# Performance work log

Hardware: AMD Instinct MI355X
Metric: run time of the kernel (lower is better)

The kernel has to match this reference:

```python
import jax, jax.numpy as jnp
import numpy as np

EPS = 1e-5
NEG = -1000000.0
H = 8

def layer_norm(v, g, b):
    mu = jnp.mean(v, axis=-1, keepdims=True)
    var = jnp.var(v, axis=-1, keepdims=True)
    return (v - mu) * jax.lax.rsqrt(var + EPS) * g + b

def setup_inputs() -> dict:
    key = jax.random.key(0)
    ks = jax.random.split(key, 12)
    B, T, Tc, D, Dc = 8, 2048, 512, 1024, 512
    s = lambda fan: 1.0 / np.sqrt(fan)
    return {
        'query': jax.random.normal(ks[0], (B, T, D), jnp.float32),
        'x': jax.random.normal(ks[1], (B, T, D), jnp.float32),
        'cond_emb': jax.random.normal(ks[2], (B, Tc, Dc), jnp.float32),
        'src_mask': jax.random.uniform(ks[3], (B, T, 1), jnp.float32),
        'cond_mask': jax.random.uniform(ks[4], (B, Tc, 1), jnp.float32),
        'norm_x_g': jnp.ones((D,), jnp.float32),
        'norm_x_b': jnp.zeros((D,), jnp.float32),
        'norm_c_g': jnp.ones((Dc,), jnp.float32),
        'norm_c_b': jnp.zeros((Dc,), jnp.float32),
        'W_kc': jax.random.normal(ks[5], (D, Dc), jnp.float32) * s(Dc),
        'b_kc': jnp.zeros((D,), jnp.float32),
        'W_vc': jax.random.normal(ks[6], (D, Dc), jnp.float32) * s(Dc),
        'b_vc': jnp.zeros((D,), jnp.float32),
        'W_kx': jax.random.normal(ks[7], (D, D), jnp.float32) * s(D),
        'b_kx': jnp.zeros((D,), jnp.float32),
        'W_vx': jax.random.normal(ks[8], (D, D), jnp.float32) * s(D),
        'b_vx': jnp.zeros((D,), jnp.float32),
        'W_y': jax.random.normal(ks[9], (D, D), jnp.float32) * s(D),
        'b_y': jnp.zeros((D,), jnp.float32),
    }

def reference(query, x, cond_emb, src_mask, cond_mask,
              norm_x_g, norm_x_b, norm_c_g, norm_c_b,
              W_kc, b_kc, W_vc, b_vc, W_kx, b_kx, W_vx, b_vx, W_y, b_y):
    B, T, D = x.shape
    Tc = cond_emb.shape[1]
    N = T + Tc
    xn = layer_norm(x, norm_x_g, norm_x_b)          # (B,T,D)
    cn = layer_norm(cond_emb, norm_c_g, norm_c_b)   # (B,Tc,Dc)
    # keys with additive mask penalty, concatenated over sequence dim
    k_cond = cn @ W_kc.T + b_kc + (1.0 - cond_mask) * NEG
    k_x = xn @ W_kx.T + b_kx + (1.0 - src_mask) * NEG
    key = jnp.concatenate([k_cond, k_x], axis=1)    # (B,N,D)
    q = jax.nn.softmax(query.reshape(B, T, H, D // H), axis=-1)
    k = jax.nn.softmax(key.reshape(B, N, H, D // H), axis=1)
    v_cond = (cn @ W_vc.T + b_vc) * cond_mask
    v_x = (xn @ W_vx.T + b_vx) * src_mask
    v = jnp.concatenate([v_cond, v_x], axis=1).reshape(B, N, H, D // H)
    attn = jnp.einsum('bnhd,bnhl->bhdl', k, v)      # (B,H,d,d) linear-attention KV
    y = jnp.einsum('bthd,bhdl->bthl', q, attn).reshape(B, T, D)
    return y @ W_y.T + b_y
```

## Files before the change

### kernel.cpp

```cpp
#include <hip/hip_runtime.h>


typedef short s16x8 __attribute__((ext_vector_type(8)));
typedef float f32x4 __attribute__((ext_vector_type(4)));

__device__ __forceinline__ float b2f(short s) {
    unsigned int u = ((unsigned int)(unsigned short)s) << 16;
    return __uint_as_float(u);
}
__device__ __forceinline__ short f2b(float f) {
    unsigned int u = __float_as_uint(f);
    u += 0x7fffu + ((u >> 16) & 1u);
    return (short)(u >> 16);
}

typedef void __attribute__((address_space(1)))* gas_ptr;
typedef void __attribute__((address_space(3)))* las_ptr;
__device__ __forceinline__ void async_cp16(const void* g, void* l) {
    __builtin_amdgcn_global_load_lds((gas_ptr)g, (las_ptr)l, 16, 0, 0);
}

__device__ __forceinline__ float pen_of(const float* __restrict__ cmask,
                                        const float* __restrict__ smask,
                                        int b, int n) {
    float mk = (n < 512) ? cmask[b * 512 + n] : smask[b * 2048 + n - 512];
    return (1.0f - mk) * -1000000.0f;
}

__global__ __launch_bounds__(256) void cvt_all(const float* __restrict__ Wkc,
                                               const float* __restrict__ Wvc,
                                               const float* __restrict__ Wkx,
                                               const float* __restrict__ Wvx,
                                               const float* __restrict__ Wy,
                                               short* __restrict__ dst) {
    int g = (blockIdx.x * 256 + threadIdx.x) * 4;
    const float* src;
    if (g < 524288)        src = Wkc + g;
    else if (g < 1048576)  src = Wvc + (g - 524288);
    else if (g < 2097152)  src = Wkx + (g - 1048576);
    else if (g < 3145728)  src = Wvx + (g - 2097152);
    else                   src = Wy  + (g - 3145728);
    float4 v = *(const float4*)src;
    short4 o;
    o.x = f2b(v.x); o.y = f2b(v.y); o.z = f2b(v.z); o.w = f2b(v.w);
    *(short4*)&dst[g] = o;
}

__global__ __launch_bounds__(256) void ln_kernel(const float* __restrict__ x,
                                                 const float* __restrict__ g,
                                                 const float* __restrict__ be,
                                                 short* __restrict__ out, int L) {
    long row = blockIdx.x;
    const float* xr = x + row * L;
    short* orow = out + row * L;
    int tid = threadIdx.x;
    int i0 = tid * 4;
    bool active = i0 < L;
    float v0 = 0.f, v1 = 0.f, v2 = 0.f, v3 = 0.f;
    if (active) {
        float4 p = *(const float4*)&xr[i0];
        v0 = p.x; v1 = p.y; v2 = p.z; v3 = p.w;
    }
    float s = v0 + v1 + v2 + v3;
    float s2 = v0*v0 + v1*v1 + v2*v2 + v3*v3;
    #pragma unroll
    for (int off = 32; off > 0; off >>= 1) {
        s  += __shfl_down(s, off);
        s2 += __shfl_down(s2, off);
    }
    __shared__ float ss[4], sq[4];
    int wave = tid >> 6, lane = tid & 63;
    if (lane == 0) { ss[wave] = s; sq[wave] = s2; }
    __syncthreads();
    if (tid == 0) {
        float t1 = ss[0] + ss[1] + ss[2] + ss[3];
        float t2 = sq[0] + sq[1] + sq[2] + sq[3];
        float mu = t1 / (float)L;
        float var = t2 / (float)L - mu * mu;
        ss[0] = mu;
        sq[0] = rsqrtf(var + 1e-5f);
    }
    __syncthreads();
    float mu = ss[0], rs = sq[0];
    if (active) {
        float4 gp = *(const float4*)&g[i0];
        float4 bp = *(const float4*)&be[i0];
        short4 o;
        o.x = f2b((v0 - mu) * rs * gp.x + bp.x);
        o.y = f2b((v1 - mu) * rs * gp.y + bp.y);
        o.z = f2b((v2 - mu) * rs * gp.z + bp.z);
        o.w = f2b((v3 - mu) * rs * gp.w + bp.w);
        *(short4*)&orow[i0] = o;
    }
}

__global__ __launch_bounds__(256) void qsoftmax_kernel(const float* __restrict__ q,
                                                       short* __restrict__ out) {
    long row = (long)blockIdx.x * 4 + (threadIdx.x >> 6);
    int lane = threadIdx.x & 63;
    const float* qr = q + row * 128;
    float2 p = *(const float2*)&qr[lane * 2];
    float v0 = p.x, v1 = p.y;
    float m = fmaxf(v0, v1);
    #pragma unroll
    for (int off = 32; off > 0; off >>= 1) m = fmaxf(m, __shfl_xor(m, off));
    float e0 = __expf(v0 - m), e1 = __expf(v1 - m);
    float s = e0 + e1;
    #pragma unroll
    for (int off = 32; off > 0; off >>= 1) s += __shfl_xor(s, off);
    float inv = 1.0f / s;
    short2 o; o.x = f2b(e0 * inv); o.y = f2b(e1 * inv);
    *(short2*)&out[row * 128 + lane * 2] = o;
}

__global__ __launch_bounds__(256) void kstats1(const short* __restrict__ klog,
                                               const float* __restrict__ cmask,
                                               const float* __restrict__ smask,
                                               float* __restrict__ partM,
                                               float* __restrict__ partS) {
    int c = blockIdx.x * 256 + threadIdx.x;
    int b = blockIdx.y;
    int n0 = blockIdx.z * 256;
    const short* base = klog + (long)b * 2560 * 1024 + c;
    float m = -3.4e38f, s = 0.f;
    for (int k = 0; k < 256; ++k) {
        int n = n0 + k;
        float v = b2f(base[(long)n * 1024]) + pen_of(cmask, smask, b, n);
        float nm = fmaxf(m, v);
        s = s * __expf(m - nm) + __expf(v - nm);
        m = nm;
    }
    long o = ((long)(b * 10 + blockIdx.z)) * 1024 + c;
    partM[o] = m;
    partS[o] = s;
}

__global__ __launch_bounds__(256) void kstats2(const float* __restrict__ partM,
                                               const float* __restrict__ partS,
                                               float* __restrict__ Ms,
                                               float* __restrict__ iSs) {
    int c = blockIdx.x * 256 + threadIdx.x;
    int b = blockIdx.y;
    float M = -3.4e38f;
    #pragma unroll
    for (int k = 0; k < 10; ++k)
        M = fmaxf(M, partM[((long)(b * 10 + k)) * 1024 + c]);
    float S = 0.f;
    #pragma unroll
    for (int k = 0; k < 10; ++k) {
        long o = ((long)(b * 10 + k)) * 1024 + c;
        S += partS[o] * __expf(partM[o] - M);
    }
    Ms[b * 1024 + c] = M;
    iSs[b * 1024 + c] = 1.0f / S;
}

template<int MODE>
__global__ __launch_bounds__(256) void gemm_bt(
        const short* __restrict__ A, int lda, long strideA,
        const short* __restrict__ B, int ldb,
        void* __restrict__ OutA, void* __restrict__ OutB,
        int ldo, long strideO,
        int K,
        const float* __restrict__ biasK, const float* __restrict__ biasV,
        const float* __restrict__ mask, long strideMask) {
    __shared__ short As[128 * 64];
    __shared__ short Bs[128 * 64];
    int tid = threadIdx.x;
    int wave = tid >> 6, lane = tid & 63;
    int n0 = blockIdx.x * 128;
    int m0 = blockIdx.y * 128;
    int z = blockIdx.z;

    const short* Ab;
    const short* Bb;
    if (MODE == 2) {
        Ab = A + (z & 7) * 128;
        Bb = B + (long)z * 16384;
    } else if (MODE == 4) {
        Ab = A + (long)z * strideA;
        Bb = B + (long)z * 1048576;
    } else {
        Ab = A + (long)z * strideA;
        Bb = B;
    }

    f32x4 acc[4][4];
    #pragma unroll
    for (int i = 0; i < 4; ++i)
        #pragma unroll
        for (int j = 0; j < 4; ++j) {
            f32x4 zz = {0.f, 0.f, 0.f, 0.f};
            acc[i][j] = zz;
        }

    int wm = wave >> 1, wn = wave & 1;
    int r = lane & 15, q = lane >> 4;

    for (int k0 = 0; k0 < K; k0 += 64) {
        __syncthreads();
        #pragma unroll
        for (int it = 0; it < 4; ++it) {
            int cid = it * 256 + tid;
            int row = cid >> 3;
            int c8  = cid & 7;
            int col = ((c8 ^ (row & 7)) << 3);
            const short* ga = Ab + (long)(m0 + row) * lda + k0 + col;
            const short* gb = Bb + (long)(n0 + row) * ldb + k0 + col;
            async_cp16(ga, &As[cid * 8]);
            async_cp16(gb, &Bs[cid * 8]);
        }
        __syncthreads();
        #pragma unroll
        for (int kk = 0; kk < 64; kk += 32) {
            s16x8 af[4], bfr[4];
            #pragma unroll
            for (int i = 0; i < 4; ++i) {
                int rowA = wm * 64 + i * 16 + r;
                int rowB = wn * 64 + i * 16 + r;
                int ch = (kk >> 3) + q;
                af[i]  = *(const s16x8*)&As[rowA * 64 + ((ch ^ (rowA & 7)) << 3)];
                bfr[i] = *(const s16x8*)&Bs[rowB * 64 + ((ch ^ (rowB & 7)) << 3)];
            }
            #pragma unroll
            for (int i = 0; i < 4; ++i)
                #pragma unroll
                for (int j = 0; j < 4; ++j)
                    acc[i][j] = __builtin_amdgcn_mfma_f32_16x16x32_bf16(af[i], bfr[j], acc[i][j], 0, 0, 0);
        }
    }

    #pragma unroll
    for (int i = 0; i < 4; ++i) {
        int gmb = m0 + wm * 64 + i * 16 + q * 4;
        #pragma unroll
        for (int j = 0; j < 4; ++j) {
            int gn = n0 + wn * 64 + j * 16 + r;
            #pragma unroll
            for (int rg = 0; rg < 4; ++rg) {
                int row = gmb + rg;
                float v = acc[i][j][rg];
                if (MODE == 0) {
                    if (gn < 1024) {
                        ((short*)OutA)[(long)z * strideO + (long)row * ldo + gn] =
                            f2b(v + biasK[gn]);
                    } else {
                        int gv = gn - 1024;
                        float mk = mask[(long)z * strideMask + row];
                        ((short*)OutB)[(long)z * strideO + (long)row * ldo + gv] =
                            f2b((v + biasV[gv]) * mk);
                    }
                } else if (MODE == 2) {
                    ((short*)OutA)[(long)(z >> 3) * 1048576 + (long)row * 1024 +
                                   (z & 7) * 128 + gn] = f2b(v);
                } else {
                    ((float*)OutA)[(long)z * strideO + (long)row * ldo + gn] =
                        v + biasK[gn];
                }
            }
        }
    }
}

template<int MODE>
__global__ __launch_bounds__(512, 2) void gemm256(
        const short* __restrict__ A, int lda, long strideA,
        const short* __restrict__ B, int ldb,
        void* __restrict__ OutA, void* __restrict__ OutB,
        int ldo, long strideO,
        int K,
        const float* __restrict__ biasK, const float* __restrict__ biasV,
        const float* __restrict__ mask, long strideMask) {
    extern __shared__ short lds[];
    int tid = threadIdx.x;
    int wave = tid >> 6, lane = tid & 63;
    int n0 = blockIdx.x * 256;
    int m0 = blockIdx.y * 256;
    int z = blockIdx.z;

    const short* Ab;
    const short* Bb;
    if (MODE == 4) {
        Ab = A + (long)z * strideA;
        Bb = B + (long)z * 1048576;
    } else {
        Ab = A + (long)z * strideA;
        Bb = B;
    }

    f32x4 acc[8][4];
    #pragma unroll
    for (int i = 0; i < 8; ++i)
        #pragma unroll
        for (int j = 0; j < 4; ++j) {
            f32x4 zz = {0.f, 0.f, 0.f, 0.f};
            acc[i][j] = zz;
        }

    int wm = wave >> 2, wn = wave & 3;
    int r = lane & 15, q = lane >> 4;

    auto stage = [&](int buf, int k0) {
        short* dstb = lds + buf * 32768;
        #pragma unroll
        for (int it = 0; it < 8; ++it) {
            int cid = it * 512 + tid;
            int rid = cid & 2047;
            int row = rid >> 3;
            int c8  = rid & 7;
            int col = ((c8 ^ (row & 7)) << 3);
            const short* g = (cid < 2048)
                ? (Ab + (long)(m0 + row) * lda + k0 + col)
                : (Bb + (long)(n0 + row) * ldb + k0 + col);
            async_cp16(g, dstb + cid * 8);
        }
    };

    auto compute = [&](int buf) {
        const short* Asb = lds + buf * 32768;
        const short* Bsb = Asb + 16384;
        s16x8 bfr[2][4];
        #pragma unroll
        for (int kk2 = 0; kk2 < 2; ++kk2)
            #pragma unroll
            for (int j = 0; j < 4; ++j) {
                int rowB = wn * 64 + j * 16 + r;
                int ch = kk2 * 4 + q;
                bfr[kk2][j] = *(const s16x8*)&Bsb[rowB * 64 + ((ch ^ (rowB & 7)) << 3)];
            }
        __builtin_amdgcn_s_setprio(1);
        #pragma unroll
        for (int i = 0; i < 8; ++i) {
            int rowA = wm * 128 + i * 16 + r;
            s16x8 a0 = *(const s16x8*)&Asb[rowA * 64 + (((q    ) ^ (rowA & 7)) << 3)];
            s16x8 a1 = *(const s16x8*)&Asb[rowA * 64 + (((q + 4) ^ (rowA & 7)) << 3)];
            #pragma unroll
            for (int j = 0; j < 4; ++j)
                acc[i][j] = __builtin_amdgcn_mfma_f32_16x16x32_bf16(a0, bfr[0][j], acc[i][j], 0, 0, 0);
            #pragma unroll
            for (int j = 0; j < 4; ++j)
                acc[i][j] = __builtin_amdgcn_mfma_f32_16x16x32_bf16(a1, bfr[1][j], acc[i][j], 0, 0, 0);
        }
        __builtin_amdgcn_s_setprio(0);
    };

    int nt = K >> 6;
    stage(0, 0);
    __syncthreads();
    for (int t = 0; t < nt; ++t) {
        if (t + 1 < nt) stage((t + 1) & 1, (t + 1) << 6);
        compute(t & 1);
        __syncthreads();
    }

    #pragma unroll
    for (int i = 0; i < 8; ++i) {
        int gmb = m0 + wm * 128 + i * 16 + q * 4;
        #pragma unroll
        for (int j = 0; j < 4; ++j) {
            int gn = n0 + wn * 64 + j * 16 + r;
            #pragma unroll
            for (int rg = 0; rg < 4; ++rg) {
                int row = gmb + rg;
                float v = acc[i][j][rg];
                if (MODE == 0) {
                    if (gn < 1024) {
                        ((short*)OutA)[(long)z * strideO + (long)row * ldo + gn] =
                            f2b(v + biasK[gn]);
                    } else {
                        int gv = gn - 1024;
                        float mk = mask[(long)z * strideMask + row];
                        ((short*)OutB)[(long)z * strideO + (long)row * ldo + gv] =
                            f2b((v + biasV[gv]) * mk);
                    }
                } else {
                    ((float*)OutA)[(long)z * strideO + (long)row * ldo + gn] =
                        v + biasK[gn];
                }
            }
        }
    }
}

__global__ __launch_bounds__(256) void attn_part(const short* __restrict__ klog,
                                                 const short* __restrict__ vbuf,
                                                 const float* __restrict__ cmask,
                                                 const float* __restrict__ smask,
                                                 const float* __restrict__ Ms,
                                                 float* __restrict__ pbuf) {
    __shared__ short kT[128 * 64];
    __shared__ short vT[128 * 64];
    int ns = blockIdx.x;
    int z = blockIdx.y;
    int b = z >> 3, h = z & 7;
    int tid = threadIdx.x;
    int wave = tid >> 6, lane = tid & 63;
    int r = lane & 15, q = lane >> 4;
    int wm = wave >> 1, wn = wave & 1;

    int cg = h * 128 + lane * 2;
    float M0 = Ms[b * 1024 + cg];
    float M1 = Ms[b * 1024 + cg + 1];

    f32x4 acc[4][4];
    #pragma unroll
    for (int i = 0; i < 4; ++i)
        #pragma unroll
        for (int j = 0; j < 4; ++j) {
            f32x4 zz = {0.f, 0.f, 0.f, 0.f};
            acc[i][j] = zz;
        }

    long base = ((long)b * 2560) * 1024 + h * 128;
    int nbase = ns * 320;
    int swz = (lane & 7) << 3;
    for (int n0 = 0; n0 < 320; n0 += 64) {
        __syncthreads();
        #pragma unroll 4
        for (int i = 0; i < 16; ++i) {
            int nl = i * 4 + wave;
            int n = nbase + n0 + nl;
            float pen = pen_of(cmask, smask, b, n);
            long g = base + (long)n * 1024 + lane * 2;
            short2 k2 = *(const short2*)&klog[g];
            short2 v2 = *(const short2*)&vbuf[g];
            float w0 = __expf(b2f(k2.x) + pen - M0);
            float w1 = __expf(b2f(k2.y) + pen - M1);
            int c = lane * 2;
            int sw = nl ^ swz;
            kT[c * 64 + sw] = f2b(w0);
            kT[(c + 1) * 64 + sw] = f2b(w1);
            vT[c * 64 + sw] = v2.x;
            vT[(c + 1) * 64 + sw] = v2.y;
        }
        __syncthreads();
        #pragma unroll
        for (int kk = 0; kk < 64; kk += 32) {
            s16x8 af[4], bfr[4];
            #pragma unroll
            for (int i = 0; i < 4; ++i) {
                int cA = wm * 64 + i * 16 + r;
                int cB = wn * 64 + i * 16 + r;
                af[i]  = *(const s16x8*)&kT[cA * 64 + ((kk + q * 8) ^ (((cA >> 1) & 7) << 3))];
                bfr[i] = *(const s16x8*)&vT[cB * 64 + ((kk + q * 8) ^ (((cB >> 1) & 7) << 3))];
            }
            #pragma unroll
            for (int i = 0; i < 4; ++i)
                #pragma unroll
                for (int j = 0; j < 4; ++j)
                    acc[i][j] = __builtin_amdgcn_mfma_f32_16x16x32_bf16(af[i], bfr[j], acc[i][j], 0, 0, 0);
        }
    }
    float* outp = pbuf + ((long)z * 8 + ns) * 16384;
    #pragma unroll
    for (int i = 0; i < 4; ++i) {
        int d0 = wm * 64 + i * 16 + q * 4;
        #pragma unroll
        for (int j = 0; j < 4; ++j) {
            int l = wn * 64 + j * 16 + r;
            *(f32x4*)&outp[l * 128 + d0] = acc[i][j];
        }
    }
}

__global__ __launch_bounds__(256) void reduce_attn(const float* __restrict__ pbuf,
                                                   const float* __restrict__ iSs,
                                                   short* __restrict__ attnD) {
    int idx = blockIdx.x * 256 + threadIdx.x;
    int z = idx >> 14, rem = idx & 16383;
    int d = rem & 127, l = rem >> 7;
    int b = z >> 3, h = z & 7;
    const float* p = pbuf + (long)z * 8 * 16384 + rem;
    float s = 0.f;
    #pragma unroll
    for (int ns = 0; ns < 8; ++ns) s += p[ns * 16384];
    attnD[(long)z * 16384 + d * 128 + l] = f2b(s * iSs[b * 1024 + h * 128 + d]);
}

extern "C" void kernel_launch(void* const* d_in, const int* in_sizes, int n_in,
                              void* d_out, int out_size, void* d_ws, size_t ws_size,
                              hipStream_t stream) {
    const float* query = (const float*)d_in[0];
    const float* x     = (const float*)d_in[1];
    const float* cond  = (const float*)d_in[2];
    const float* smask = (const float*)d_in[3];
    const float* cmask = (const float*)d_in[4];
    const float* gx  = (const float*)d_in[5];
    const float* bx  = (const float*)d_in[6];
    const float* gc  = (const float*)d_in[7];
    const float* bc  = (const float*)d_in[8];
    const float* Wkc = (const float*)d_in[9];
    const float* bkc = (const float*)d_in[10];
    const float* Wvc = (const float*)d_in[11];
    const float* bvc = (const float*)d_in[12];
    const float* Wkx = (const float*)d_in[13];
    const float* bkx = (const float*)d_in[14];
    const float* Wvx = (const float*)d_in[15];
    const float* bvx = (const float*)d_in[16];
    const float* Wy  = (const float*)d_in[17];
    const float* by  = (const float*)d_in[18];

    size_t o_xn    = 0;
    size_t o_cn    = o_xn    + 33554432;
    size_t o_klog  = o_cn    + 4194304;
    size_t o_vbuf  = o_klog  + 41943040;
    size_t o_qsm   = o_vbuf  + 41943040;
    size_t o_attnD = o_qsm   + 33554432;
    size_t o_partM = o_attnD + 2097152;
    size_t o_partS = o_partM + 327680;
    size_t o_Ms    = o_partS + 327680;
    size_t o_iSs   = o_Ms    + 32768;
    size_t o_wkc   = o_iSs   + 32768;
    size_t o_wvc   = o_wkc   + 1048576;
    size_t o_wkx   = o_wvc   + 1048576;
    size_t o_wvx   = o_wkx   + 2097152;
    size_t o_wy    = o_wvx   + 2097152;
    size_t need    = o_wy    + 2097152;
    if (ws_size < need) return;

    char* w = (char*)d_ws;
    short* xn    = (short*)(w + o_xn);
    short* cn    = (short*)(w + o_cn);
    short* klog  = (short*)(w + o_klog);
    short* vbuf  = (short*)(w + o_vbuf);
    short* qsm   = (short*)(w + o_qsm);
    short* attnD = (short*)(w + o_attnD);
    float* partM = (float*)(w + o_partM);
    float* partS = (float*)(w + o_partS);
    float* Ms    = (float*)(w + o_Ms);
    float* iSs   = (float*)(w + o_iSs);
    short* wkc   = (short*)(w + o_wkc);
    short* wkx   = (short*)(w + o_wkx);
    short* wy    = (short*)(w + o_wy);
    float* pbuf  = (float*)xn;
    short* Zt    = klog;

    static bool attr_set = false;
    if (!attr_set) {
        (void)hipFuncSetAttribute((const void*)gemm256<0>,
                                  hipFuncAttributeMaxDynamicSharedMemorySize, 131072);
        (void)hipFuncSetAttribute((const void*)gemm256<4>,
                                  hipFuncAttributeMaxDynamicSharedMemorySize, 131072);
        attr_set = true;
    }

    cvt_all<<<4096, 256, 0, stream>>>(Wkc, Wvc, Wkx, Wvx, Wy, wkc);

    ln_kernel<<<16384, 256, 0, stream>>>(x, gx, bx, xn, 1024);
    ln_kernel<<<4096, 256, 0, stream>>>(cond, gc, bc, cn, 512);
    qsoftmax_kernel<<<32768, 256, 0, stream>>>(query, qsm);

    gemm256<0><<<dim3(8, 8, 8), 512, 131072, stream>>>(
        xn, 1024, 2097152L, wkx, 1024,
        klog + 512 * 1024, vbuf + 512 * 1024, 1024, 2621440L,
        1024, bkx, bvx, smask, 2048L);
    gemm_bt<0><<<dim3(16, 4, 8), 256, 0, stream>>>(
        cn, 512, 262144L, wkc, 512,
        klog, vbuf, 1024, 2621440L,
        512, bkc, bvc, cmask, 512L);

    kstats1<<<dim3(4, 8, 10), 256, 0, stream>>>(klog, cmask, smask, partM, partS);
    kstats2<<<dim3(4, 8), 256, 0, stream>>>(partM, partS, Ms, iSs);

    attn_part<<<dim3(8, 64), 256, 0, stream>>>(klog, vbuf, cmask, smask, Ms, pbuf);
    reduce_attn<<<4096, 256, 0, stream>>>(pbuf, iSs, attnD);

    gemm_bt<2><<<dim3(1, 8, 64), 256, 0, stream>>>(
        wy, 1024, 0L, attnD, 128,
        Zt, nullptr, 1024, 0L,
        128, nullptr, nullptr, nullptr, 0L);
    gemm256<4><<<dim3(4, 8, 8), 512, 131072, stream>>>(
        qsm, 1024, 2097152L, Zt, 1024,
        d_out, nullptr, 1024, 2097152L,
        1024, by, nullptr, nullptr, 0L);
}
```

Baseline: 500.0 us.

## Pipeline GEMMs with 4-stage async LDS ring and XCD-aware block remap

Both GEMM kernels move from a one- or two-buffer K=64 loop to a four-buffer ring of K=32 slices. Three slices are prefetched ahead, and each step uses a manual vmcnt wait plus barrier instead of __syncthreads. Block indices are remapped so neighbouring tiles land on the same XCD, which should improve L2 reuse. The LDS layout packs two rows per swizzled row, and address offsets are precomputed once. This trades more LDS per block and fragile hand-counted waitcnt logic for better overlap of loads with MFMA work.

```diff
diff --git a/kernel.cpp b/kernel.cpp
--- a/kernel.cpp
+++ b/kernel.cpp
@@ -25,6 +25,17 @@
                                         int b, int n) {
     float mk = (n < 512) ? cmask[b * 512 + n] : smask[b * 2048 + n - 512];
     return (1.0f - mk) * -1000000.0f;
+}
+
+__device__ __forceinline__ void xcd_remap(int& gx, int& gy, int& gz) {
+    int lb = blockIdx.x + gridDim.x * (blockIdx.y + gridDim.y * blockIdx.z);
+    int nx = gridDim.x;
+    int gpx = (gridDim.y * gridDim.z) >> 3;
+    int xcd = lb & 7, rest = lb >> 3;
+    gx = rest % nx;
+    int gidx = xcd * gpx + rest / nx;
+    gy = gidx % gridDim.y;
+    gz = gidx / gridDim.y;
 }
 
 __global__ __launch_bounds__(256) void cvt_all(const float* __restrict__ Wkc,
@@ -164,13 +175,14 @@
         int K,
         const float* __restrict__ biasK, const float* __restrict__ biasV,
         const float* __restrict__ mask, long strideMask) {
-    __shared__ short As[128 * 64];
-    __shared__ short Bs[128 * 64];
+    __shared__ short lds[4 * 8192];
     int tid = threadIdx.x;
     int wave = tid >> 6, lane = tid & 63;
-    int n0 = blockIdx.x * 128;
-    int m0 = blockIdx.y * 128;
-    int z = blockIdx.z;
+    int bx, by, bz;
+    xcd_remap(bx, by, bz);
+    int n0 = bx * 128;
+    int m0 = by * 128;
+    int z = bz;
 
     const short* Ab;
     const short* Bb;
@@ -197,37 +209,79 @@
     int wm = wave >> 1, wn = wave & 1;
     int r = lane & 15, q = lane >> 4;
 
-    for (int k0 = 0; k0 < K; k0 += 64) {
-        __syncthreads();
+    const short* sp0; const short* sp1; const short* sp2; const short* sp3;
+    int lo0, lo1, lo2, lo3;
+    {
         #pragma unroll
         for (int it = 0; it < 4; ++it) {
             int cid = it * 256 + tid;
-            int row = cid >> 3;
-            int c8  = cid & 7;
-            int col = ((c8 ^ (row & 7)) << 3);
-            const short* ga = Ab + (long)(m0 + row) * lda + k0 + col;
-            const short* gb = Bb + (long)(n0 + row) * ldb + k0 + col;
-            async_cp16(ga, &As[cid * 8]);
-            async_cp16(gb, &Bs[cid * 8]);
-        }
-        __syncthreads();
-        #pragma unroll
-        for (int kk = 0; kk < 64; kk += 32) {
-            s16x8 af[4], bfr[4];
+            int rid = cid & 511;
+            int srow = rid >> 3;
+            int scol = rid & 7;
+            int scol0 = scol ^ (srow & 7);
+            int row = srow * 2 + (scol0 >> 2);
+            int col = (scol0 & 3) << 3;
+            const short* p = (cid < 512)
+                ? (Ab + (long)(m0 + row) * lda + col)
+                : (Bb + (long)(n0 + row) * ldb + col);
+            int lo = cid * 8;
+            if (it == 0) { sp0 = p; lo0 = lo; }
+            else if (it == 1) { sp1 = p; lo1 = lo; }
+            else if (it == 2) { sp2 = p; lo2 = lo; }
+            else { sp3 = p; lo3 = lo; }
+        }
+    }
+
+    int offA[4], offB[4];
+    #pragma unroll
+    for (int i = 0; i < 4; ++i) {
+        int rowA = wm * 64 + i * 16 + r;
+        int srow = rowA >> 1;
+        int slot = ((((rowA & 1) << 2) | q) ^ (srow & 7));
+        offA[i] = srow * 64 + slot * 8;
+        int rowB = wn * 64 + i * 16 + r;
+        int srowB = rowB >> 1;
+        int slotB = ((((rowB & 1) << 2) | q) ^ (srowB & 7));
+        offB[i] = 4096 + srowB * 64 + slotB * 8;
+    }
+
+    int nt = K >> 5;
+    #pragma unroll
+    for (int pt = 0; pt < 3; ++pt) {
+        async_cp16(sp0 + (pt << 5), &lds[pt * 8192 + lo0]);
+        async_cp16(sp1 + (pt << 5), &lds[pt * 8192 + lo1]);
+        async_cp16(sp2 + (pt << 5), &lds[pt * 8192 + lo2]);
+        async_cp16(sp3 + (pt << 5), &lds[pt * 8192 + lo3]);
+    }
+
+    for (int t = 0; t < nt; ++t) {
+        if (t + 2 < nt)
+            asm volatile("s_waitcnt vmcnt(8)\n\ts_barrier" ::: "memory");
+        else if (t + 1 < nt)
+            asm volatile("s_waitcnt vmcnt(4)\n\ts_barrier" ::: "memory");
+        else
+            asm volatile("s_waitcnt vmcnt(0)\n\ts_barrier" ::: "memory");
+        const short* base = &lds[(t & 3) * 8192];
+        s16x8 af[4], bfr[4];
+        #pragma unroll
+        for (int j = 0; j < 4; ++j) bfr[j] = *(const s16x8*)&base[offB[j]];
+        #pragma unroll
+        for (int i = 0; i < 4; ++i) af[i] = *(const s16x8*)&base[offA[i]];
+        if (t + 3 < nt) {
+            int buf = (t + 3) & 3;
+            int ks = (t + 3) << 5;
+            async_cp16(sp0 + ks, &lds[buf * 8192 + lo0]);
+            async_cp16(sp1 + ks, &lds[buf * 8192 + lo1]);
+            async_cp16(sp2 + ks, &lds[buf * 8192 + lo2]);
+            async_cp16(sp3 + ks, &lds[buf * 8192 + lo3]);
+        }
+        __builtin_amdgcn_s_setprio(1);
+        #pragma unroll
+        for (int i = 0; i < 4; ++i)
             #pragma unroll
-            for (int i = 0; i < 4; ++i) {
-                int rowA = wm * 64 + i * 16 + r;
-                int rowB = wn * 64 + i * 16 + r;
-                int ch = (kk >> 3) + q;
-                af[i]  = *(const s16x8*)&As[rowA * 64 + ((ch ^ (rowA & 7)) << 3)];
-                bfr[i] = *(const s16x8*)&Bs[rowB * 64 + ((ch ^ (rowB & 7)) << 3)];
-            }
-            #pragma unroll
-            for (int i = 0; i < 4; ++i)
-                #pragma unroll
-                for (int j = 0; j < 4; ++j)
-                    acc[i][j] = __builtin_amdgcn_mfma_f32_16x16x32_bf16(af[i], bfr[j], acc[i][j], 0, 0, 0);
-        }
+            for (int j = 0; j < 4; ++j)
+                acc[i][j] = __builtin_amdgcn_mfma_f32_16x16x32_bf16(af[i], bfr[j], acc[i][j], 0, 0, 0);
+        __builtin_amdgcn_s_setprio(0);
     }
 
     #pragma unroll
@@ -274,9 +328,11 @@
     extern __shared__ short lds[];
     int tid = threadIdx.x;
     int wave = tid >> 6, lane = tid & 63;
-    int n0 = blockIdx.x * 256;
-    int m0 = blockIdx.y * 256;
-    int z = blockIdx.z;
+    int bx, by, bz;
+    xcd_remap(bx, by, bz);
+    int n0 = bx * 256;
+    int m0 = by * 256;
+    int z = bz;
 
     const short* Ab;
     const short* Bb;
@@ -300,57 +356,82 @@
     int wm = wave >> 2, wn = wave & 3;
     int r = lane & 15, q = lane >> 4;
 
-    auto stage = [&](int buf, int k0) {
-        short* dstb = lds + buf * 32768;
-        #pragma unroll
-        for (int it = 0; it < 8; ++it) {
+    const short* sp0; const short* sp1; const short* sp2; const short* sp3;
+    int lo0, lo1, lo2, lo3;
+    {
+        #pragma unroll
+        for (int it = 0; it < 4; ++it) {
             int cid = it * 512 + tid;
-            int rid = cid & 2047;
-            int row = rid >> 3;
-            int c8  = rid & 7;
-            int col = ((c8 ^ (row & 7)) << 3);
-            const short* g = (cid < 2048)
-                ? (Ab + (long)(m0 + row) * lda + k0 + col)
-                : (Bb + (long)(n0 + row) * ldb + k0 + col);
-            async_cp16(g, dstb + cid * 8);
-        }
-    };
-
-    auto compute = [&](int buf) {
-        const short* Asb = lds + buf * 32768;
-        const short* Bsb = Asb + 16384;
-        s16x8 bfr[2][4];
-        #pragma unroll
-        for (int kk2 = 0; kk2 < 2; ++kk2)
-            #pragma unroll
-            for (int j = 0; j < 4; ++j) {
-                int rowB = wn * 64 + j * 16 + r;
-                int ch = kk2 * 4 + q;
-                bfr[kk2][j] = *(const s16x8*)&Bsb[rowB * 64 + ((ch ^ (rowB & 7)) << 3)];
-            }
+            int rid = cid & 1023;
+            int srow = rid >> 3;
+            int scol = rid & 7;
+            int scol0 = scol ^ (srow & 7);
+            int row = srow * 2 + (scol0 >> 2);
+            int col = (scol0 & 3) << 3;
+            const short* p = (cid < 1024)
+                ? (Ab + (long)(m0 + row) * lda + col)
+                : (Bb + (long)(n0 + row) * ldb + col);
+            int lo = cid * 8;
+            if (it == 0) { sp0 = p; lo0 = lo; }
+            else if (it == 1) { sp1 = p; lo1 = lo; }
+            else if (it == 2) { sp2 = p; lo2 = lo; }
+            else { sp3 = p; lo3 = lo; }
+        }
+    }
+
+    int offA[8], offB[4];
+    #pragma unroll
+    for (int i = 0; i < 8; ++i) {
+        int rowA = wm * 128 + i * 16 + r;
+        int srow = rowA >> 1;
+        int slot = ((((rowA & 1) << 2) | q) ^ (srow & 7));
+        offA[i] = srow * 64 + slot * 8;
+    }
+    #pragma unroll
+    for (int j = 0; j < 4; ++j) {
+        int rowB = wn * 64 + j * 16 + r;
+        int srow = rowB >> 1;
+        int slot = ((((rowB & 1) << 2) | q) ^ (srow & 7));
+        offB[j] = 8192 + srow * 64 + slot * 8;
+    }
+
+    int nt = K >> 5;
+    #pragma unroll
+    for (int pt = 0; pt < 3; ++pt) {
+        async_cp16(sp0 + (pt << 5), &lds[pt * 16384 + lo0]);
+        async_cp16(sp1 + (pt << 5), &lds[pt * 16384 + lo1]);
+        async_cp16(sp2 + (pt << 5), &lds[pt * 16384 + lo2]);
+        async_cp16(sp3 + (pt << 5), &lds[pt * 16384 + lo3]);
+    }
+
+    for (int t = 0; t < nt; ++t) {
+        if (t + 2 < nt)
+            asm volatile("s_waitcnt vmcnt(8)\n\ts_barrier" ::: "memory");
+        else if (t + 1 < nt)
+            asm volatile("s_waitcnt vmcnt(4)\n\ts_barrier" ::: "memory");
+        else
+            asm volatile("s_waitcnt vmcnt(0)\n\ts_barrier" ::: "memory");
+        const short* base = &lds[(t & 3) * 16384];
+        s16x8 af[8], bfr[4];
+        #pragma unroll
+        for (int j = 0; j < 4; ++j) bfr[j] = *(const s16x8*)&base[offB[j]];
+        #pragma unroll
+        for (int i = 0; i < 8; ++i) af[i] = *(const s16x8*)&base[offA[i]];
+        if (t + 3 < nt) {
+            int buf = (t + 3) & 3;
+            int ks = (t + 3) << 5;
+            async_cp16(sp0 + ks, &lds[buf * 16384 + lo0]);
+            async_cp16(sp1 + ks, &lds[buf * 16384 + lo1]);
+            async_cp16(sp2 + ks, &lds[buf * 16384 + lo2]);
+            async_cp16(sp3 + ks, &lds[buf * 16384 + lo3]);
+        }
         __builtin_amdgcn_s_setprio(1);
         #pragma unroll
-        for (int i = 0; i < 8; ++i) {
-            int rowA = wm * 128 + i * 16 + r;
-            s16x8 a0 = *(const s16x8*)&Asb[rowA * 64 + (((q    ) ^ (rowA & 7)) << 3)];
-            s16x8 a1 = *(const s16x8*)&Asb[rowA * 64 + (((q + 4) ^ (rowA & 7)) << 3)];
+        for (int i = 0; i < 8; ++i)
             #pragma unroll
             for (int j = 0; j < 4; ++j)
-                acc[i][j] = __builtin_amdgcn_mfma_f32_16x16x32_bf16(a0, bfr[0][j], acc[i][j], 0, 0, 0);
-            #pragma unroll
-            for (int j = 0; j < 4; ++j)
-                acc[i][j] = __builtin_amdgcn_mfma_f32_16x16x32_bf16(a1, bfr[1][j], acc[i][j], 0, 0, 0);
-        }
+                acc[i][j] = __builtin_amdgcn_mfma_f32_16x16x32_bf16(af[i], bfr[j], acc[i][j], 0, 0, 0);
         __builtin_amdgcn_s_setprio(0);
-    };
-
-    int nt = K >> 6;
-    stage(0, 0);
-    __syncthreads();
-    for (int t = 0; t < nt; ++t) {
-        if (t + 1 < nt) stage((t + 1) & 1, (t + 1) << 6);
-        compute(t & 1);
-        __syncthreads();
     }
 
     #pragma unroll
```

Measured after the change: 489.8 us. 2.0% less time.
